# Kernel tuning notes

Measured on AMD Instinct MI355X. Metric: run time of the kernel, lower is better.

The kernel has to match this reference:

```python
import jax, jax.numpy as jnp
import numpy as np

N = 100_000
E = 1_600_000
D_IN, D_HID, D_OUT = 512, 256, 256


def setup_inputs() -> dict:
    key = jax.random.key(0)
    ks = jax.random.split(key, 10)
    x = jax.random.normal(ks[0], (N, D_IN), dtype=jnp.float32)
    edge_index = jax.random.randint(ks[1], (2, E), 0, N, dtype=jnp.int64)
    edge_weight = jax.random.uniform(ks[2], (E,), dtype=jnp.float32)
    # Glorot-ish init for the per-layer linear weights (PyG GCNConv: Linear w/o bias, bias added after aggregation)
    W1 = jax.random.normal(ks[3], (D_IN, D_HID), dtype=jnp.float32) * (1.0 / np.sqrt(D_IN))
    b1 = jnp.zeros((D_HID,), dtype=jnp.float32)
    W2 = jax.random.normal(ks[4], (D_HID, D_HID), dtype=jnp.float32) * (1.0 / np.sqrt(D_HID))
    b2 = jnp.zeros((D_HID,), dtype=jnp.float32)
    W3 = jax.random.normal(ks[5], (D_HID, D_OUT), dtype=jnp.float32) * (1.0 / np.sqrt(D_HID))
    b3 = jnp.zeros((D_OUT,), dtype=jnp.float32)
    return {"x": x, "edge_index": edge_index, "edge_weight": edge_weight,
            "W1": W1, "b1": b1, "W2": W2, "b2": b2, "W3": W3, "b3": b3}


def gcn_layer(h_in, W, b, row, col, ew, n):
    # PyG GCNConv with normalize=True, add_self_loops=True (fill value 1.0), aggr='add':
    # h = X W; deg[i] = sum of incoming edge weights (incl. self loop);
    # norm_e = deg^-1/2[row] * w_e * deg^-1/2[col]; out[col] += norm_e * h[row]; out += bias
    h = h_in @ W                                            # [n, d_out]
    deg = jnp.zeros((n,), h.dtype).at[col].add(ew) + 1.0    # +1 from self loop
    dinv = jnp.where(deg > 0, jax.lax.rsqrt(deg), 0.0)      # deg_inv_sqrt, inf -> 0
    norm = dinv[row] * ew * dinv[col]                       # [E]
    out = jnp.zeros_like(h).at[col].add(norm[:, None] * h[row])
    out = out + (dinv * dinv)[:, None] * h                  # self-loop contribution (norm_ii = dinv_i^2)
    return out + b


def reference(x, edge_index, edge_weight, W1, b1, W2, b2, W3, b3):
    row, col = edge_index[0], edge_index[1]
    n = x.shape[0]
    # dropout p=0.0 -> identity
    h = jax.nn.relu(gcn_layer(x, W1, b1, row, col, edge_weight, n))
    h = jax.nn.relu(gcn_layer(h, W2, b2, row, col, edge_weight, n))
    return gcn_layer(h, W3, b3, row, col, edge_weight, n)
```

## Files before the change

kernel.cpp:

```cpp
#include <hip/hip_runtime.h>
#include <hip/hip_bf16.h>


#define D 256
#define ELLW 48
#define BSH2 9
#define NB2MAX 256
#define DEPTH 24
#define GCAP 8960
#define FIXSCALE 1099511627776.0f
#define FIXINV   9.094947017729282e-13

typedef unsigned short ushort_t;
typedef unsigned long long u64;
typedef float f32x2 __attribute__((ext_vector_type(2)));
typedef float f32x4 __attribute__((ext_vector_type(4)));
typedef short bf16x8 __attribute__((ext_vector_type(8)));
typedef unsigned int u32x4 __attribute__((ext_vector_type(4)));

__device__ __forceinline__ float blo(unsigned u) { return __uint_as_float(u << 16); }
__device__ __forceinline__ float bhi(unsigned u) { return __uint_as_float(u & 0xFFFF0000u); }
__device__ __forceinline__ ushort_t f2b(float f) {
    unsigned u = __float_as_uint(f);
    return (ushort_t)((u + 0x7FFFu + ((u >> 16) & 1u)) >> 16);
}
__device__ __forceinline__ void gload_lds16(const ushort_t* g, ushort_t* l) {
    __builtin_amdgcn_global_load_lds((const __attribute__((address_space(1))) unsigned int*)g,
                                     (__attribute__((address_space(3))) unsigned int*)l, 16, 0, 0);
}

__global__ void zero_gfill(int* __restrict__ gfill, int nb) {
    if ((int)threadIdx.x < nb) gfill[threadIdx.x] = 0;
}

__global__ __launch_bounds__(1024) void bin_p1(const int* __restrict__ row,
                                               const int* __restrict__ col,
                                               const float* __restrict__ ew,
                                               int* __restrict__ gfill,
                                               u64* __restrict__ bins, int E, int nb) {
    __shared__ u64 lbuf[196][DEPTH];
    __shared__ int lcnt[196];
    const int t = threadIdx.x;
    if (t < 196) lcnt[t] = 0;
    __syncthreads();
    int per = (E + gridDim.x - 1) / gridDim.x;
    int e0 = blockIdx.x * per;
    int e1 = e0 + per;
    if (e1 > E) e1 = E;
    for (int base = e0; base < e1; base += 1024) {
        int e = base + t;
        if (e < e1) {
            int c = __builtin_nontemporal_load(&col[e]);
            int r = __builtin_nontemporal_load(&row[e]);
            float w = __builtin_nontemporal_load(&ew[e]);
            int b = c >> BSH2;
            u64 rec = ((u64)__float_as_uint(w) << 32) | ((u64)(unsigned)r << 9) |
                      (unsigned)(c & ((1 << BSH2) - 1));
            int pos = atomicAdd(&lcnt[b], 1);
            if (pos < DEPTH) {
                lbuf[b][pos] = rec;
            } else {
                int gp = atomicAdd(&gfill[b], 1);
                if (gp < GCAP) bins[(size_t)b * GCAP + gp] = rec;
                atomicSub(&lcnt[b], 1);
            }
        }
        __syncthreads();
        if (t < nb) {
            int c = lcnt[t];
            int k8 = c & ~7;
            if (k8 > 0) {
                int gp = atomicAdd(&gfill[t], k8);
                for (int i = 0; i < k8; ++i)
                    if (gp + i < GCAP) bins[(size_t)t * GCAP + gp + i] = lbuf[t][i];
                int rem = c - k8;
                for (int i = 0; i < rem; ++i) lbuf[t][i] = lbuf[t][k8 + i];
                lcnt[t] = rem;
            }
        }
        __syncthreads();
    }
    if (t < nb) {
        int c = lcnt[t];
        if (c > 0) {
            int gp = atomicAdd(&gfill[t], c);
            for (int i = 0; i < c; ++i)
                if (gp + i < GCAP) bins[(size_t)t * GCAP + gp + i] = lbuf[t][i];
        }
    }
}

__global__ __launch_bounds__(512) void bin_p2(const u64* __restrict__ bins,
                                              const int* __restrict__ gfill,
                                              int* __restrict__ cnt,
                                              float* __restrict__ dinv,
                                              u64* __restrict__ ell, int N) {
    __shared__ u64 sacc[1 << BSH2];
    const int b = blockIdx.x, t = threadIdx.x;
    const int base = b << BSH2;
    for (int i = t; i < (1 << BSH2); i += 512) sacc[i] = 0ull;
    __syncthreads();
    int fill = gfill[b];
    if (fill > GCAP) fill = GCAP;
    for (int i = t; i < fill; i += 512) {
        u64 rec = bins[(size_t)b * GCAP + i];
        int li = (int)(rec & ((1 << BSH2) - 1));
        unsigned r = (unsigned)((rec >> 9) & 0x1FFFFu);
        unsigned wb = (unsigned)(rec >> 32);
        u64 pack = (1ull << 48) | (u64)(__uint_as_float(wb) * FIXSCALE);
        int pos = (int)(atomicAdd(&sacc[li], pack) >> 48);
        if (pos < ELLW)
            ell[(size_t)(base + li) * ELLW + pos] = ((u64)wb << 32) | r;
    }
    __syncthreads();
    for (int i = t; i < (1 << BSH2); i += 512) {
        int node = base + i;
        if (node < N) {
            u64 p = sacc[i];
            int m = (int)(p >> 48);
            cnt[node] = (m > ELLW) ? ELLW : m;
            float sum = (float)((double)(p & 0xFFFFFFFFFFFFull) * FIXINV);
            dinv[node] = rsqrtf(sum + 1.0f);
        }
    }
}

__global__ __launch_bounds__(256) void norm_ell(const int* __restrict__ cnt,
                                                const float* __restrict__ dinv,
                                                u64* __restrict__ ell, int N) {
    int node = blockIdx.x * 4 + (threadIdx.x >> 6);
    if (node >= N) return;
    int lane = threadIdx.x & 63;
    int m = cnt[node];
    if (lane < m) {
        u64 r = ell[(size_t)node * ELLW + lane];
        int src = (int)(unsigned)r;
        float w = __uint_as_float((unsigned)(r >> 32));
        float nrm = dinv[src] * w * dinv[node];
        ell[(size_t)node * ELLW + lane] = ((u64)__float_as_uint(nrm) << 32) | (unsigned)src;
    }
}

__global__ __launch_bounds__(256) void cvtT_kernel(const float* __restrict__ W,
                                                   ushort_t* __restrict__ WT, int K, int C) {
    int i = blockIdx.x * 256 + threadIdx.x;
    if (i < K * C) {
        int c = i / K, k = i - c * K;
        WT[i] = f2b(W[(size_t)k * C + c]);
    }
}

template <int K, bool AF32>
__global__ __launch_bounds__(256) void gemm_mfma(const void* __restrict__ Ap,
                                                 const ushort_t* __restrict__ WT,
                                                 ushort_t* __restrict__ C, int nvalid) {
    __shared__ ushort_t As[128 * 64];
    __shared__ ushort_t Bs[256 * 64];
    const int tid = threadIdx.x;
    const int lane = tid & 63, wave = tid >> 6;
    const int wrow = wave >> 1, wcol = wave & 1;
    const int fr = lane & 15, fq = lane >> 4;
    const int r0 = blockIdx.x * 128;

    f32x4 acc[4][8] = {};

    for (int k0 = 0; k0 < K; k0 += 64) {
        if constexpr (AF32) {
            const float* Af = (const float*)Ap;
#pragma unroll
            for (int i = 0; i < 8; ++i) {
                int idx = i * 256 + tid;
                int rowt = idx >> 4;
                int c4 = idx & 15;
                int grow = r0 + rowt;
                if (grow >= nvalid) grow = nvalid - 1;
                f32x4 v = __builtin_nontemporal_load(
                    (const f32x4*)&Af[(size_t)grow * K + k0 + c4 * 4]);
                __hip_bfloat162 b01 = __float22bfloat162_rn(make_float2(v[0], v[1]));
                __hip_bfloat162 b23 = __float22bfloat162_rn(make_float2(v[2], v[3]));
                uint2 st = make_uint2(*(unsigned*)&b01, *(unsigned*)&b23);
                int slot = c4 >> 1, half = c4 & 1;
                int off = rowt * 64 + ((slot ^ (rowt & 7)) << 3) + (half << 2);
                *(uint2*)&As[off] = st;
            }
        } else {
            const ushort_t* Ab = (const ushort_t*)Ap;
#pragma unroll
            for (int q = 0; q < 4; ++q) {
                int qa = wave * 4 + q;
                int rowt = qa * 8 + (lane >> 3);
                int g = (lane & 7) ^ (lane >> 3);
                gload_lds16(&Ab[(size_t)(r0 + rowt) * K + k0 + g * 8], &As[qa * 512]);
            }
        }
#pragma unroll
        for (int q = 0; q < 8; ++q) {
            int qb = wave * 8 + q;
            int rowt = qb * 8 + (lane >> 3);
            int g = (lane & 7) ^ (lane >> 3);
            gload_lds16(&WT[(size_t)rowt * K + k0 + g * 8], &Bs[qb * 512]);
        }
        __syncthreads();

#pragma unroll
        for (int kk = 0; kk < 2; ++kk) {
            int g = (kk * 4 + fq) ^ (fr & 7);
            bf16x8 aF[4];
#pragma unroll
            for (int m = 0; m < 4; ++m) {
                int arow = wrow * 64 + m * 16 + fr;
                aF[m] = *(const bf16x8*)&As[arow * 64 + g * 8];
            }
#pragma unroll
            for (int n = 0; n < 8; ++n) {
                int bcol = wcol * 128 + n * 16 + fr;
                bf16x8 bF = *(const bf16x8*)&Bs[bcol * 64 + g * 8];
#pragma unroll
                for (int m = 0; m < 4; ++m)
                    acc[m][n] = __builtin_amdgcn_mfma_f32_16x16x32_bf16(
                        bF, aF[m], acc[m][n], 0, 0, 0);
            }
        }
        __syncthreads();
    }

#pragma unroll
    for (int m = 0; m < 4; ++m) {
        int gr = r0 + wrow * 64 + m * 16 + fr;
        if (gr < nvalid) {
#pragma unroll
            for (int n = 0; n < 8; ++n) {
                ushort4 h;
                h.x = f2b(acc[m][n][0]); h.y = f2b(acc[m][n][1]);
                h.z = f2b(acc[m][n][2]); h.w = f2b(acc[m][n][3]);
                *(ushort4*)&C[(size_t)gr * D + wcol * 128 + n * 16 + fq * 4] = h;
            }
        }
    }
}

template <bool RELU, bool OUTF32>
__global__ __launch_bounds__(256) void agg_kernel(const ushort_t* __restrict__ hb,
                                                  const float* __restrict__ dinv,
                                                  const float* __restrict__ bias,
                                                  const int* __restrict__ cnt,
                                                  const u64* __restrict__ ell,
                                                  void* __restrict__ outp, int N) {
    int node = blockIdx.x * 4 + (threadIdx.x >> 6);
    if (node >= N) return;
    int lane = threadIdx.x & 63;
    int half = lane >> 5;
    int fl = lane & 31;
    float dn = dinv[node], d2 = dn * dn;

    u32x4 sv = *(const u32x4*)&hb[(size_t)node * 256 + fl * 8];
    float sc = half ? 0.f : d2;
    float a0 = sc * blo(sv.x), a1 = sc * bhi(sv.x);
    float a2 = sc * blo(sv.y), a3 = sc * bhi(sv.y);
    float a4 = sc * blo(sv.z), a5 = sc * bhi(sv.z);
    float a6 = sc * blo(sv.w), a7 = sc * bhi(sv.w);

    int m = cnt[node];
    int srcl = 0;
    float wl = 0.f;
    if (lane < m) {
        u64 r = __builtin_nontemporal_load(&ell[(size_t)node * ELLW + lane]);
        srcl = (int)(unsigned)r;
        wl = __uint_as_float((unsigned)(r >> 32));
    }
    int steps = (m + 1) >> 1;
#pragma unroll 8
    for (int j = 0; j < steps; ++j) {
        int idx2 = 2 * j + half;
        int src = __shfl(srcl, idx2);
        float w = __shfl(wl, idx2);
        u32x4 v = *(const u32x4*)&hb[(size_t)src * 256 + fl * 8];
        a0 = fmaf(w, blo(v.x), a0); a1 = fmaf(w, bhi(v.x), a1);
        a2 = fmaf(w, blo(v.y), a2); a3 = fmaf(w, bhi(v.y), a3);
        a4 = fmaf(w, blo(v.z), a4); a5 = fmaf(w, bhi(v.z), a5);
        a6 = fmaf(w, blo(v.w), a6); a7 = fmaf(w, bhi(v.w), a7);
    }
    a0 += __shfl_xor(a0, 32); a1 += __shfl_xor(a1, 32);
    a2 += __shfl_xor(a2, 32); a3 += __shfl_xor(a3, 32);
    a4 += __shfl_xor(a4, 32); a5 += __shfl_xor(a5, 32);
    a6 += __shfl_xor(a6, 32); a7 += __shfl_xor(a7, 32);
    float r0 = half ? a4 : a0;
    float r1 = half ? a5 : a1;
    float r2 = half ? a6 : a2;
    float r3 = half ? a7 : a3;
    f32x4 bb = *(const f32x4*)&bias[fl * 8 + half * 4];
    r0 += bb[0]; r1 += bb[1]; r2 += bb[2]; r3 += bb[3];
    if (RELU) {
        r0 = fmaxf(r0, 0.f); r1 = fmaxf(r1, 0.f);
        r2 = fmaxf(r2, 0.f); r3 = fmaxf(r3, 0.f);
    }
    if (OUTF32) {
        f32x4 o = {r0, r1, r2, r3};
        __builtin_nontemporal_store(
            o, (f32x4*)((float*)outp + (size_t)node * 256 + fl * 8 + half * 4));
    } else {
        u64 p = (u64)f2b(r0) | ((u64)f2b(r1) << 16) | ((u64)f2b(r2) << 32) | ((u64)f2b(r3) << 48);
        __builtin_nontemporal_store(
            p, (u64*)((ushort_t*)outp + (size_t)node * 256 + fl * 8 + half * 4));
    }
}

extern "C" void kernel_launch(void* const* d_in, const int* in_sizes, int n_in,
                              void* d_out, int out_size, void* d_ws, size_t ws_size,
                              hipStream_t stream) {
    const float* x  = (const float*)d_in[0];
    const int*   ei = (const int*)d_in[1];
    const float* ew = (const float*)d_in[2];
    const float* W1 = (const float*)d_in[3];
    const float* b1 = (const float*)d_in[4];
    const float* W2 = (const float*)d_in[5];
    const float* b2 = (const float*)d_in[6];
    const float* W3 = (const float*)d_in[7];
    const float* b3 = (const float*)d_in[8];
    const int N = in_sizes[0] / 512;
    const int E = in_sizes[2];
    const int* row = ei;
    const int* col = ei + E;
    float* out = (float*)d_out;

    const int MB = (N + 127) / 128;
    const size_t Npad = (size_t)MB * 128;
    const int NB2 = (N + (1 << BSH2) - 1) >> BSH2;

    char* ws = (char*)d_ws;
    size_t off = 0;
    auto alloc = [&](size_t bytes) -> void* {
        void* p = ws + off;
        off += (bytes + 255) / 256 * 256;
        return p;
    };
    ushort_t* hb  = (ushort_t*)alloc(Npad * D * sizeof(ushort_t));
    u64*      ell = (u64*)alloc((size_t)N * ELLW * sizeof(u64));
    ushort_t* WT1 = (ushort_t*)alloc((size_t)512 * D * sizeof(ushort_t));
    ushort_t* WT2 = (ushort_t*)alloc((size_t)256 * D * sizeof(ushort_t));
    ushort_t* WT3 = (ushort_t*)alloc((size_t)256 * D * sizeof(ushort_t));
    int*   cnt    = (int*)alloc((size_t)N * sizeof(int));
    float* dinv   = (float*)alloc((size_t)N * sizeof(float));
    int*   gfill  = (int*)alloc((size_t)NB2MAX * sizeof(int));
    u64*   bins   = (u64*)hb;
    ushort_t* ab  = (ushort_t*)d_out;

    int gA = (N + 3) / 4;
    zero_gfill<<<1, 256, 0, stream>>>(gfill, NB2);
    cvtT_kernel<<<(512 * D + 255) / 256, 256, 0, stream>>>(W1, WT1, 512, D);
    cvtT_kernel<<<(256 * D + 255) / 256, 256, 0, stream>>>(W2, WT2, 256, D);
    cvtT_kernel<<<(256 * D + 255) / 256, 256, 0, stream>>>(W3, WT3, 256, D);
    bin_p1<<<256, 1024, 0, stream>>>(row, col, ew, gfill, bins, E, NB2);
    bin_p2<<<NB2, 512, 0, stream>>>(bins, gfill, cnt, dinv, ell, N);
    norm_ell<<<gA, 256, 0, stream>>>(cnt, dinv, ell, N);

    gemm_mfma<512, true><<<MB, 256, 0, stream>>>(x, WT1, hb, N);
    agg_kernel<true, false><<<gA, 256, 0, stream>>>(hb, dinv, b1, cnt, ell, ab, N);
    gemm_mfma<256, false><<<MB, 256, 0, stream>>>(ab, WT2, hb, N);
    agg_kernel<true, false><<<gA, 256, 0, stream>>>(hb, dinv, b2, cnt, ell, ab, N);
    gemm_mfma<256, false><<<MB, 256, 0, stream>>>(ab, WT3, hb, N);
    agg_kernel<false, true><<<gA, 256, 0, stream>>>(hb, dinv, b3, cnt, ell, out, N);
}
```

Baseline: 656.0 us.

## Fuse edge normalization into first aggregation and parallelize bin flush per wave

Drops the separate norm_ell pass. The first aggregation kernel now computes dinv[src]*w*dinv[node] for each edge and writes the normalized weight back into the ELL array, where the later layers read it. Separately, the bin_p1 flush used one serial thread per bin; it now gives each bin to a wave, so lanes copy the records in parallel and one lane does the atomic. This saves a kernel launch and a full read/write pass over the ELL array, at the cost of extra scattered dinv loads and writes inside layer 1's aggregation.

```diff
diff --git a/kernel.cpp b/kernel.cpp
--- a/kernel.cpp
+++ b/kernel.cpp
@@ -41,6 +41,7 @@
     __shared__ u64 lbuf[196][DEPTH];
     __shared__ int lcnt[196];
     const int t = threadIdx.x;
+    const int wv = t >> 6, ln = t & 63;
     if (t < 196) lcnt[t] = 0;
     __syncthreads();
     int per = (E + gridDim.x - 1) / gridDim.x;
@@ -66,26 +67,35 @@
             }
         }
         __syncthreads();
-        if (t < nb) {
-            int c = lcnt[t];
+        for (int b = wv; b < nb; b += 16) {
+            int c = lcnt[b];
             int k8 = c & ~7;
             if (k8 > 0) {
-                int gp = atomicAdd(&gfill[t], k8);
-                for (int i = 0; i < k8; ++i)
-                    if (gp + i < GCAP) bins[(size_t)t * GCAP + gp + i] = lbuf[t][i];
+                int gp = 0;
+                if (ln == 0) gp = atomicAdd(&gfill[b], k8);
+                gp = __shfl(gp, 0);
+                if (ln < k8) {
+                    int idx = gp + ln;
+                    if (idx < GCAP) bins[(size_t)b * GCAP + idx] = lbuf[b][ln];
+                }
                 int rem = c - k8;
-                for (int i = 0; i < rem; ++i) lbuf[t][i] = lbuf[t][k8 + i];
-                lcnt[t] = rem;
+                u64 mv = (ln < rem) ? lbuf[b][k8 + ln] : 0ull;
+                if (ln < rem) lbuf[b][ln] = mv;
+                if (ln == 0) lcnt[b] = rem;
             }
         }
         __syncthreads();
     }
-    if (t < nb) {
-        int c = lcnt[t];
+    for (int b = wv; b < nb; b += 16) {
+        int c = lcnt[b];
         if (c > 0) {
-            int gp = atomicAdd(&gfill[t], c);
-            for (int i = 0; i < c; ++i)
-                if (gp + i < GCAP) bins[(size_t)t * GCAP + gp + i] = lbuf[t][i];
+            int gp = 0;
+            if (ln == 0) gp = atomicAdd(&gfill[b], c);
+            gp = __shfl(gp, 0);
+            if (ln < c) {
+                int idx = gp + ln;
+                if (idx < GCAP) bins[(size_t)b * GCAP + idx] = lbuf[b][ln];
+            }
         }
     }
 }
@@ -125,22 +135,6 @@
     }
 }
 
-__global__ __launch_bounds__(256) void norm_ell(const int* __restrict__ cnt,
-                                                const float* __restrict__ dinv,
-                                                u64* __restrict__ ell, int N) {
-    int node = blockIdx.x * 4 + (threadIdx.x >> 6);
-    if (node >= N) return;
-    int lane = threadIdx.x & 63;
-    int m = cnt[node];
-    if (lane < m) {
-        u64 r = ell[(size_t)node * ELLW + lane];
-        int src = (int)(unsigned)r;
-        float w = __uint_as_float((unsigned)(r >> 32));
-        float nrm = dinv[src] * w * dinv[node];
-        ell[(size_t)node * ELLW + lane] = ((u64)__float_as_uint(nrm) << 32) | (unsigned)src;
-    }
-}
-
 __global__ __launch_bounds__(256) void cvtT_kernel(const float* __restrict__ W,
                                                    ushort_t* __restrict__ WT, int K, int C) {
     int i = blockIdx.x * 256 + threadIdx.x;
@@ -239,12 +233,12 @@
     }
 }
 
-template <bool RELU, bool OUTF32>
+template <bool NORM, bool RELU, bool OUTF32>
 __global__ __launch_bounds__(256) void agg_kernel(const ushort_t* __restrict__ hb,
                                                   const float* __restrict__ dinv,
                                                   const float* __restrict__ bias,
                                                   const int* __restrict__ cnt,
-                                                  const u64* __restrict__ ell,
+                                                  u64* __restrict__ ell,
                                                   void* __restrict__ outp, int N) {
     int node = blockIdx.x * 4 + (threadIdx.x >> 6);
     if (node >= N) return;
@@ -264,9 +258,16 @@
     int srcl = 0;
     float wl = 0.f;
     if (lane < m) {
-        u64 r = __builtin_nontemporal_load(&ell[(size_t)node * ELLW + lane]);
+        u64 r = ell[(size_t)node * ELLW + lane];
         srcl = (int)(unsigned)r;
-        wl = __uint_as_float((unsigned)(r >> 32));
+        float w = __uint_as_float((unsigned)(r >> 32));
+        if (NORM) {
+            wl = dinv[srcl] * w * dn;
+            ell[(size_t)node * ELLW + lane] =
+                ((u64)__float_as_uint(wl) << 32) | (unsigned)srcl;
+        } else {
+            wl = w;
+        }
     }
     int steps = (m + 1) >> 1;
 #pragma unroll 8
@@ -352,12 +353,11 @@
     cvtT_kernel<<<(256 * D + 255) / 256, 256, 0, stream>>>(W3, WT3, 256, D);
     bin_p1<<<256, 1024, 0, stream>>>(row, col, ew, gfill, bins, E, NB2);
     bin_p2<<<NB2, 512, 0, stream>>>(bins, gfill, cnt, dinv, ell, N);
-    norm_ell<<<gA, 256, 0, stream>>>(cnt, dinv, ell, N);
 
     gemm_mfma<512, true><<<MB, 256, 0, stream>>>(x, WT1, hb, N);
-    agg_kernel<true, false><<<gA, 256, 0, stream>>>(hb, dinv, b1, cnt, ell, ab, N);
+    agg_kernel<true, true, false><<<gA, 256, 0, stream>>>(hb, dinv, b1, cnt, ell, ab, N);
     gemm_mfma<256, false><<<MB, 256, 0, stream>>>(ab, WT2, hb, N);
-    agg_kernel<true, false><<<gA, 256, 0, stream>>>(hb, dinv, b2, cnt, ell, ab, N);
+    agg_kernel<false, true, false><<<gA, 256, 0, stream>>>(hb, dinv, b2, cnt, ell, ab, N);
     gemm_mfma<256, false><<<MB, 256, 0, stream>>>(ab, WT3, hb, N);
-    agg_kernel<false, true><<<gA, 256, 0, stream>>>(hb, dinv, b3, cnt, ell, out, N);
-}
+    agg_kernel<false, false, true><<<gA, 256, 0, stream>>>(hb, dinv, b3, cnt, ell, out, N);
+}
```

Measured after the change: 980.2 us. 49.4% more time.
